# Kernel tuning notes

Measured on AMD Instinct MI355X. Metric: run time of the kernel, lower is better.

## Reference

```python
import jax, jax.numpy as jnp
import numpy as np


def setup_inputs() -> dict:
    key = jax.random.key(0)
    kq, kk, kv = jax.random.split(key, 3)
    shape = (2, 16, 2048, 64)  # [B, H, S, D]
    return {
        "q": jax.random.normal(kq, shape, dtype=jnp.float32),
        "k": jax.random.normal(kk, shape, dtype=jnp.float32),
        "v": jax.random.normal(kv, shape, dtype=jnp.float32),
    }


def reference(q, k, v):
    # scores = q @ k^T / sqrt(d_k)  -> [B, H, S, S]
    d_k = k.shape[-1]
    scale = 1.0 / jnp.sqrt(jnp.asarray(d_k, dtype=q.dtype))
    scores = jnp.einsum("bhqd,bhkd->bhqk", q, k) * scale
    seq_len = q.shape[-2]
    # causal mask: position q attends to k <= q
    causal = jnp.tril(jnp.ones((seq_len, seq_len), dtype=bool))
    scores = jnp.where(causal, scores, jnp.asarray(-jnp.inf, dtype=scores.dtype))
    probs = jax.nn.softmax(scores, axis=-1)
    return jnp.einsum("bhqk,bhkd->bhqd", probs, v)
```

## Files before the change

### kernel.cpp

```cpp
#include <hip/hip_runtime.h>
#include <hip/hip_bf16.h>

typedef short bf16x8 __attribute__((ext_vector_type(8)));
typedef short bf16x4 __attribute__((ext_vector_type(4)));
typedef float f32x4  __attribute__((ext_vector_type(4)));
typedef float f32x16 __attribute__((ext_vector_type(16)));

#define D_DIM 64
#define SEQ 2048
#define BHD (SEQ * D_DIM)
#define SCALE_L2E 0.1803368801111204f

__device__ __forceinline__ unsigned short f2bf(float f) {
    unsigned u = __builtin_bit_cast(unsigned, f);
    u += 0x7fffu + ((u >> 16) & 1u);
    return (unsigned short)(u >> 16);
}
__device__ __forceinline__ unsigned swz(unsigned row, unsigned colByte) {
    return (row * 128u + colByte) ^ ((row & 7u) << 4);
}
__device__ __forceinline__ void gl_lds(const unsigned short* g, unsigned char* lds_generic,
                                       unsigned lds_off) {
    __builtin_amdgcn_global_load_lds(
        (const __attribute__((address_space(1))) void*)g,
        (__attribute__((address_space(3))) void*)(lds_generic + lds_off), 16, 0, 0);
}
__device__ __forceinline__ float fexp2(float x) {
    float r; asm("v_exp_f32 %0, %1" : "=v"(r) : "v"(x)); return r;
}
__device__ __forceinline__ unsigned cvtpk(float lo, float hi) {
    unsigned r; asm("v_cvt_pk_bf16_f32 %0, %1, %2" : "=v"(r) : "v"(lo), "v"(hi)); return r;
}

__global__ __launch_bounds__(256) void prep_kernel(const float* __restrict__ K,
                                                   const float* __restrict__ V,
                                                   unsigned short* __restrict__ Kb,
                                                   unsigned short* __restrict__ Vt) {
    __shared__ unsigned short t[64][66];
    const int st = blockIdx.x;
    const int bh = blockIdx.y;
    const int tid = threadIdx.x;
    const size_t base = (size_t)bh * BHD;

    const float* ksrc = K + base + st * 4096;
    unsigned short* kdst = Kb + base + st * 4096;
    #pragma unroll
    for (int j = 0; j < 2; ++j) {
        int e = (j * 256 + tid) * 8;
        float4 a = *(const float4*)(ksrc + e);
        float4 b = *(const float4*)(ksrc + e + 4);
        bf16x8 o;
        o[0] = (short)f2bf(a.x); o[1] = (short)f2bf(a.y);
        o[2] = (short)f2bf(a.z); o[3] = (short)f2bf(a.w);
        o[4] = (short)f2bf(b.x); o[5] = (short)f2bf(b.y);
        o[6] = (short)f2bf(b.z); o[7] = (short)f2bf(b.w);
        *(bf16x8*)(kdst + e) = o;
    }

    const float* vb = V + base + st * 64 * D_DIM;
    #pragma unroll
    for (int j = 0; j < 4; ++j) {
        int n = tid + 256 * j;
        int r = n >> 4;
        int c = (n & 15) << 2;
        float4 v = *(const float4*)(vb + r * D_DIM + c);
        t[r][c + 0] = f2bf(v.x); t[r][c + 1] = f2bf(v.y);
        t[r][c + 2] = f2bf(v.z); t[r][c + 3] = f2bf(v.w);
    }
    __syncthreads();
    #pragma unroll
    for (int j = 0; j < 2; ++j) {
        int m = tid + 256 * j;
        int d = m >> 3;
        int s8 = (m & 7) << 3;
        bf16x8 o;
        #pragma unroll
        for (int e = 0; e < 8; ++e) o[e] = (short)t[s8 + e][d];
        *(bf16x8*)(Vt + base + (size_t)d * SEQ + st * 64 + s8) = o;
    }
}

__global__ __launch_bounds__(512, 4) void attn_fwd(const float* __restrict__ Qp,
                                                   const unsigned short* __restrict__ Kb,
                                                   const unsigned short* __restrict__ Vtb,
                                                   float* __restrict__ Op) {
    __shared__ __align__(16) unsigned char lds[65536];

    int id = blockIdx.y * gridDim.x + blockIdx.x;
    int j  = id >> 3;
    const int bh = (id & 7) * 4 + (j >> 4);
    const int jq = j & 15;
    const int qtile = (j < 32) ? (15 - jq) : jq;

    const int tid  = threadIdx.x;
    const int w    = tid >> 6;
    const int lane = tid & 63;
    const int l31  = lane & 31;
    const int hi2  = lane >> 5;
    const int wsub = w & 3;
    const int par  = w >> 2;

    const int qlo = qtile * 128 + wsub * 32;
    const int t_w = qlo >> 6;
    const int qg  = qlo + l31;
    const int nt  = qtile + 1;

    const size_t base = (size_t)bh * BHD;
    const float* qp = Qp + base;
    const unsigned short* kb = Kb + base;
    const unsigned short* vt = Vtb + base;
    float* op = Op + base;

    const int srow = tid >> 3;
    const int scb  = ((tid & 7) << 4) ^ ((srow & 7) << 4);
    const int kOff = srow * D_DIM + (scb >> 1);
    const int vOff = srow * SEQ + (scb >> 1);
    const unsigned sdst = (unsigned)tid * 16u;

    auto STAGE = [&](int it) {
        unsigned bb = (unsigned)(it & 1) * 32768u;
        const unsigned short* kg = kb + (size_t)(2 * it) * 4096 + kOff;
        const unsigned short* vg = vt + (size_t)(2 * it) * 64 + vOff;
        gl_lds(kg, lds, bb + sdst);
        gl_lds(vg, lds, bb + 8192u + sdst);
        gl_lds(kg + 4096, lds, bb + 16384u + sdst);
        gl_lds(vg + 64, lds, bb + 24576u + sdst);
    };

    const float* qsrc = qp + (size_t)qg * D_DIM + hi2 * 8;
    float4 qraw[8];
    #pragma unroll
    for (int dk = 0; dk < 4; ++dk) {
        qraw[2 * dk]     = *(const float4*)(qsrc + dk * 16);
        qraw[2 * dk + 1] = *(const float4*)(qsrc + dk * 16 + 4);
    }
    STAGE(0);

    bf16x8 qB[4];
    #pragma unroll
    for (int dk = 0; dk < 4; ++dk) {
        float4 a = qraw[2 * dk], b = qraw[2 * dk + 1];
        bf16x8 v;
        v[0] = (short)f2bf(a.x * SCALE_L2E); v[1] = (short)f2bf(a.y * SCALE_L2E);
        v[2] = (short)f2bf(a.z * SCALE_L2E); v[3] = (short)f2bf(a.w * SCALE_L2E);
        v[4] = (short)f2bf(b.x * SCALE_L2E); v[5] = (short)f2bf(b.y * SCALE_L2E);
        v[6] = (short)f2bf(b.z * SCALE_L2E); v[7] = (short)f2bf(b.w * SCALE_L2E);
        qB[dk] = v;
    }

    f32x16 acc0 = {}, acc1 = {};
    float m_r = -3.0e38f, l_r = 0.f;

    #pragma unroll 1
    for (int it = 0; it < nt; ++it) {
        asm volatile("s_waitcnt vmcnt(0)" ::: "memory");
        __builtin_amdgcn_s_barrier();
        __builtin_amdgcn_sched_barrier(0);
        if (it + 1 < nt) STAGE(it + 1);

        const int tile = 2 * it + par;
        if (tile <= t_w) {
            const unsigned kbuf = (unsigned)(it & 1) * 32768u + (unsigned)par * 16384u;
            const unsigned vbuf = kbuf + 8192u;

            f32x16 st0 = {}, st1 = {};
            __builtin_amdgcn_s_setprio(1);
            #pragma unroll
            for (int dk = 0; dk < 4; ++dk) {
                bf16x8 k0 = *(const bf16x8*)&lds[kbuf +
                    swz((unsigned)l31, (unsigned)(dk * 32 + hi2 * 16))];
                bf16x8 k1 = *(const bf16x8*)&lds[kbuf +
                    swz((unsigned)(32 + l31), (unsigned)(dk * 32 + hi2 * 16))];
                st0 = __builtin_amdgcn_mfma_f32_32x32x16_bf16(k0, qB[dk], st0, 0, 0, 0);
                st1 = __builtin_amdgcn_mfma_f32_32x32x16_bf16(k1, qB[dk], st1, 0, 0, 0);
            }
            __builtin_amdgcn_s_setprio(0);

            if (tile == t_w) {
                #pragma unroll
                for (int r = 0; r < 16; ++r) {
                    int kvb = tile * 64 + (r & 3) + 8 * (r >> 2) + 4 * hi2;
                    if (kvb > qg)      st0[r] = -3.0e38f;
                    if (kvb + 32 > qg) st1[r] = -3.0e38f;
                }
            }

            float m8[8];
            #pragma unroll
            for (int r = 0; r < 8; ++r)
                m8[r] = fmaxf(fmaxf(fmaxf(st0[r], st0[r + 8]), st1[r]), st1[r + 8]);
            float mx = fmaxf(fmaxf(fmaxf(m8[0], m8[1]), m8[2]),
                             fmaxf(fmaxf(m8[3], m8[4]),
                                   fmaxf(fmaxf(m8[5], m8[6]), m8[7])));

            float mn;
            if (__all(mx <= m_r + 8.0f)) {
                mn = m_r;
            } else {
                float mfull = fmaxf(mx, __shfl_xor(mx, 32));
                mn = fmaxf(m_r, mfull);
                float sc = fexp2(m_r - mn);
                m_r = mn;
                l_r *= sc;
                #pragma unroll
                for (int r = 0; r < 16; ++r) { acc0[r] *= sc; acc1[r] *= sc; }
            }

            #pragma unroll
            for (int r = 0; r < 16; ++r) st0[r] = fexp2(st0[r] - mn);
            #pragma unroll
            for (int r = 0; r < 16; ++r) st1[r] = fexp2(st1[r] - mn);
            float s16[16];
            #pragma unroll
            for (int r = 0; r < 16; ++r) s16[r] = st0[r] + st1[r];
            #pragma unroll
            for (int r = 0; r < 8; ++r) s16[r] += s16[r + 8];
            #pragma unroll
            for (int r = 0; r < 4; ++r) s16[r] += s16[r + 4];
            float rs = (s16[0] + s16[1]) + (s16[2] + s16[3]);
            rs += __shfl_xor(rs, 32);
            l_r += rs;

            bf16x8 pf[4];
            #pragma unroll
            for (int b2 = 0; b2 < 2; ++b2) {
                unsigned W[4][2];
                #pragma unroll
                for (int c = 0; c < 4; ++c) {
                    float v0 = b2 ? st1[4 * c + 0] : st0[4 * c + 0];
                    float v1 = b2 ? st1[4 * c + 1] : st0[4 * c + 1];
                    float v2 = b2 ? st1[4 * c + 2] : st0[4 * c + 2];
                    float v3 = b2 ? st1[4 * c + 3] : st0[4 * c + 3];
                    W[c][0] = cvtpk(v0, v1);
                    W[c][1] = cvtpk(v2, v3);
                }
                #pragma unroll
                for (int m = 0; m < 2; ++m) {
                    unsigned s0 = hi2 ? W[2 * m][0] : W[2 * m + 1][0];
                    unsigned s1 = hi2 ? W[2 * m][1] : W[2 * m + 1][1];
                    unsigned r0 = (unsigned)__shfl_xor((int)s0, 32);
                    unsigned r1 = (unsigned)__shfl_xor((int)s1, 32);
                    int4 fw;
                    fw.x = (int)(hi2 ? r0 : W[2 * m][0]);
                    fw.y = (int)(hi2 ? r1 : W[2 * m][1]);
                    fw.z = (int)(hi2 ? W[2 * m + 1][0] : r0);
                    fw.w = (int)(hi2 ? W[2 * m + 1][1] : r1);
                    pf[b2 * 2 + m] = __builtin_bit_cast(bf16x8, fw);
                }
            }

            __builtin_amdgcn_s_setprio(1);
            #pragma unroll
            for (int mm = 0; mm < 4; ++mm) {
                bf16x8 va0 = *(const bf16x8*)&lds[vbuf +
                    swz((unsigned)l31, (unsigned)(mm * 32 + hi2 * 16))];
                bf16x8 va1 = *(const bf16x8*)&lds[vbuf +
                    swz((unsigned)(32 + l31), (unsigned)(mm * 32 + hi2 * 16))];
                acc0 = __builtin_amdgcn_mfma_f32_32x32x16_bf16(va0, pf[mm], acc0, 0, 0, 0);
                acc1 = __builtin_amdgcn_mfma_f32_32x32x16_bf16(va1, pf[mm], acc1, 0, 0, 0);
            }
            __builtin_amdgcn_s_setprio(0);
        }
    }

    __builtin_amdgcn_s_barrier();
    const unsigned mbase = (unsigned)wsub * (64u * 144u) + (unsigned)lane * 144u;
    if (w >= 4) {
        #pragma unroll
        for (int c = 0; c < 4; ++c) {
            f32x4 q0 = {acc0[4 * c], acc0[4 * c + 1], acc0[4 * c + 2], acc0[4 * c + 3]};
            *(f32x4*)&lds[mbase + c * 16] = q0;
            f32x4 q1 = {acc1[4 * c], acc1[4 * c + 1], acc1[4 * c + 2], acc1[4 * c + 3]};
            *(f32x4*)&lds[mbase + 64 + c * 16] = q1;
        }
        *(float*)&lds[mbase + 128] = m_r;
        *(float*)&lds[mbase + 132] = l_r;
    }
    __builtin_amdgcn_s_barrier();
    if (w < 4) {
        float m2 = *(const float*)&lds[mbase + 128];
        float l2 = *(const float*)&lds[mbase + 132];
        float m  = fmaxf(m_r, m2);
        float a1 = fexp2(m_r - m);
        float a2 = fexp2(m2 - m);
        float l  = a1 * l_r + a2 * l2;
        float inv = 1.f / l;
        #pragma unroll
        for (int c = 0; c < 4; ++c) {
            f32x4 p0 = *(const f32x4*)&lds[mbase + c * 16];
            f32x4 p1 = *(const f32x4*)&lds[mbase + 64 + c * 16];
            float4 o0, o1;
            o0.x = (a1 * acc0[4 * c + 0] + a2 * p0[0]) * inv;
            o0.y = (a1 * acc0[4 * c + 1] + a2 * p0[1]) * inv;
            o0.z = (a1 * acc0[4 * c + 2] + a2 * p0[2]) * inv;
            o0.w = (a1 * acc0[4 * c + 3] + a2 * p0[3]) * inv;
            o1.x = (a1 * acc1[4 * c + 0] + a2 * p1[0]) * inv;
            o1.y = (a1 * acc1[4 * c + 1] + a2 * p1[1]) * inv;
            o1.z = (a1 * acc1[4 * c + 2] + a2 * p1[2]) * inv;
            o1.w = (a1 * acc1[4 * c + 3] + a2 * p1[3]) * inv;
            *(float4*)(op + (size_t)qg * D_DIM + 8 * c + 4 * hi2) = o0;
            *(float4*)(op + (size_t)qg * D_DIM + 32 + 8 * c + 4 * hi2) = o1;
        }
    }
}

__global__ __launch_bounds__(256) void attn_fwd_fb(
    const float* __restrict__ Qp, const float* __restrict__ Kp,
    const float* __restrict__ Vp, float* __restrict__ Op, int S)
{
    __shared__ __align__(16) unsigned char lds_k[64 * 128];
    __shared__ __align__(16) unsigned char lds_vt[64 * 128];
    __shared__ __align__(16) unsigned char lds_p[4 * 16 * 128];

    const int qt = blockIdx.x, bh = blockIdx.y, tid = threadIdx.x;
    const int w = tid >> 6, lane = tid & 63, lo = lane & 15, hi = lane >> 4;
    const size_t base = (size_t)bh * S * D_DIM;
    const float* qp = Qp + base; const float* kp = Kp + base;
    const float* vp = Vp + base; float* op = Op + base;
    const int qw = qt * 64 + w * 16;

    auto swzl = [](unsigned row, unsigned colByte) {
        return (row * 128u + colByte) ^ ((row & 7u) << 4);
    };

    bf16x8 qf[2];
    {
        const float* src = qp + (size_t)(qw + lo) * D_DIM + hi * 8;
        #pragma unroll
        for (int f = 0; f < 2; ++f) {
            float4 a = *(const float4*)(src + f * 32);
            float4 b = *(const float4*)(src + f * 32 + 4);
            bf16x8 v;
            v[0] = (short)f2bf(a.x * 0.125f); v[1] = (short)f2bf(a.y * 0.125f);
            v[2] = (short)f2bf(a.z * 0.125f); v[3] = (short)f2bf(a.w * 0.125f);
            v[4] = (short)f2bf(b.x * 0.125f); v[5] = (short)f2bf(b.y * 0.125f);
            v[6] = (short)f2bf(b.z * 0.125f); v[7] = (short)f2bf(b.w * 0.125f);
            qf[f] = v;
        }
    }
    f32x4 o_acc[4]; float m_r[4], l_r[4];
    #pragma unroll
    for (int r = 0; r < 4; ++r) { m_r[r] = -__builtin_inff(); l_r[r] = 0.f; }
    #pragma unroll
    for (int dt = 0; dt < 4; ++dt) o_acc[dt] = (f32x4){0.f, 0.f, 0.f, 0.f};
    const unsigned pbase = (unsigned)w * 2048u;

    for (int t = 0; t <= qt; ++t) {
        const size_t kv0 = (size_t)t * 64;
        __syncthreads();
        #pragma unroll
        for (int jj = 0; jj < 4; ++jj) {
            int n = tid + 256 * jj;
            int r = n >> 4, c = (n & 15) << 2;
            float4 kk = *(const float4*)(kp + (kv0 + r) * D_DIM + c);
            bf16x4 kbv;
            kbv[0] = (short)f2bf(kk.x); kbv[1] = (short)f2bf(kk.y);
            kbv[2] = (short)f2bf(kk.z); kbv[3] = (short)f2bf(kk.w);
            *(bf16x4*)&lds_k[swzl((unsigned)r, (unsigned)c * 2)] = kbv;
            float4 vv = *(const float4*)(vp + (kv0 + r) * D_DIM + c);
            *(unsigned short*)&lds_vt[swzl((unsigned)(c + 0), (unsigned)r * 2)] = f2bf(vv.x);
            *(unsigned short*)&lds_vt[swzl((unsigned)(c + 1), (unsigned)r * 2)] = f2bf(vv.y);
            *(unsigned short*)&lds_vt[swzl((unsigned)(c + 2), (unsigned)r * 2)] = f2bf(vv.z);
            *(unsigned short*)&lds_vt[swzl((unsigned)(c + 3), (unsigned)r * 2)] = f2bf(vv.w);
        }
        __syncthreads();

        float sc[4][4];
        #pragma unroll
        for (int kc = 0; kc < 4; ++kc) {
            f32x4 s = (f32x4){0.f, 0.f, 0.f, 0.f};
            #pragma unroll
            for (int f = 0; f < 2; ++f) {
                bf16x8 kfv = *(const bf16x8*)&lds_k[swzl((unsigned)(kc * 16 + lo),
                                                         (unsigned)(hi * 16 + f * 64))];
                s = __builtin_amdgcn_mfma_f32_16x16x32_bf16(qf[f], kfv, s, 0, 0, 0);
            }
            #pragma unroll
            for (int r = 0; r < 4; ++r) sc[kc][r] = s[r];
        }
        if (t == qt) {
            #pragma unroll
            for (int kc = 0; kc < 4; ++kc)
                #pragma unroll
                for (int r = 0; r < 4; ++r) {
                    int qg2 = w * 16 + hi * 4 + r, kg = kc * 16 + lo;
                    if (kg > qg2) sc[kc][r] = -__builtin_inff();
                }
        }
        float scale[4];
        #pragma unroll
        for (int r = 0; r < 4; ++r) {
            float mx = fmaxf(fmaxf(sc[0][r], sc[1][r]), fmaxf(sc[2][r], sc[3][r]));
            mx = fmaxf(mx, __shfl_xor(mx, 1)); mx = fmaxf(mx, __shfl_xor(mx, 2));
            mx = fmaxf(mx, __shfl_xor(mx, 4)); mx = fmaxf(mx, __shfl_xor(mx, 8));
            float mn = fmaxf(m_r[r], mx);
            scale[r] = __expf(m_r[r] - mn); m_r[r] = mn;
            float s0 = 0.f;
            #pragma unroll
            for (int kc = 0; kc < 4; ++kc) {
                float pv = __expf(sc[kc][r] - mn); sc[kc][r] = pv; s0 += pv;
            }
            s0 += __shfl_xor(s0, 1); s0 += __shfl_xor(s0, 2);
            s0 += __shfl_xor(s0, 4); s0 += __shfl_xor(s0, 8);
            l_r[r] = l_r[r] * scale[r] + s0;
        }
        #pragma unroll
        for (int r = 0; r < 4; ++r) {
            unsigned qr = (unsigned)(hi * 4 + r);
            #pragma unroll
            for (int kc = 0; kc < 4; ++kc)
                *(unsigned short*)&lds_p[pbase + swzl(qr, (unsigned)((kc * 16 + lo) * 2))] =
                    f2bf(sc[kc][r]);
            #pragma unroll
            for (int dt = 0; dt < 4; ++dt) o_acc[dt][r] *= scale[r];
        }
        bf16x8 pa0 = *(const bf16x8*)&lds_p[pbase + swzl((unsigned)lo, (unsigned)(hi * 16))];
        bf16x8 pa1 = *(const bf16x8*)&lds_p[pbase + swzl((unsigned)lo, (unsigned)(hi * 16 + 64))];
        #pragma unroll
        for (int dt = 0; dt < 4; ++dt) {
            bf16x8 vb0 = *(const bf16x8*)&lds_vt[swzl((unsigned)(dt * 16 + lo), (unsigned)(hi * 16))];
            bf16x8 vb1 = *(const bf16x8*)&lds_vt[swzl((unsigned)(dt * 16 + lo), (unsigned)(hi * 16 + 64))];
            o_acc[dt] = __builtin_amdgcn_mfma_f32_16x16x32_bf16(pa0, vb0, o_acc[dt], 0, 0, 0);
            o_acc[dt] = __builtin_amdgcn_mfma_f32_16x16x32_bf16(pa1, vb1, o_acc[dt], 0, 0, 0);
        }
    }
    const int qrow = qw + hi * 4;
    #pragma unroll
    for (int r = 0; r < 4; ++r) {
        float inv = 1.f / l_r[r];
        #pragma unroll
        for (int dt = 0; dt < 4; ++dt)
            op[(size_t)(qrow + r) * D_DIM + dt * 16 + lo] = o_acc[dt][r] * inv;
    }
}

extern "C" void kernel_launch(void* const* d_in, const int* in_sizes, int n_in,
                              void* d_out, int out_size, void* d_ws, size_t ws_size,
                              hipStream_t stream) {
    const float* q = (const float*)d_in[0];
    const float* k = (const float*)d_in[1];
    const float* v = (const float*)d_in[2];
    float* o = (float*)d_out;

    const size_t nelem = (size_t)32 * BHD;
    const size_t need = 2 * nelem * sizeof(unsigned short);

    if (ws_size >= need) {
        unsigned short* kbf = (unsigned short*)d_ws;
        unsigned short* vtb = kbf + nelem;
        prep_kernel<<<dim3(32, 32), 256, 0, stream>>>(k, v, kbf, vtb);
        attn_fwd<<<dim3(16, 32), 512, 0, stream>>>(q, kbf, vtb, o);
    } else {
        attn_fwd_fb<<<dim3(32, 32), 256, 0, stream>>>(q, k, v, o, SEQ);
    }
}
```

Measured before the change: 48.42 us.

## Pair complementary 64-row query tiles per 256-thread block for causal balance

Replaces the 512-thread kernel, which handled one 128-row query tile with 8 waves, by a 256-thread kernel that processes two 64-row query tiles (i and 31-i) one after the other. Pairing the tiles this way gives every block the same causal workload, which removes the tail imbalance across the 512 blocks. The cost is fewer waves per block (4 instead of 8) and per-block serialization of the two phases, including a pipeline restart and Q reload for each phase. The KV split between wave pairs and the LDS merge of partial results are kept.

```diff
diff --git a/kernel.cpp b/kernel.cpp
--- a/kernel.cpp
+++ b/kernel.cpp
@@ -80,30 +80,24 @@
     }
 }
 
-__global__ __launch_bounds__(512, 4) void attn_fwd(const float* __restrict__ Qp,
-                                                   const unsigned short* __restrict__ Kb,
-                                                   const unsigned short* __restrict__ Vtb,
-                                                   float* __restrict__ Op) {
+__global__ __launch_bounds__(256, 2) void attn_pair(const float* __restrict__ Qp,
+                                                    const unsigned short* __restrict__ Kb,
+                                                    const unsigned short* __restrict__ Vtb,
+                                                    float* __restrict__ Op) {
     __shared__ __align__(16) unsigned char lds[65536];
 
-    int id = blockIdx.y * gridDim.x + blockIdx.x;
-    int j  = id >> 3;
+    const int id = blockIdx.x;
+    const int j  = id >> 3;
     const int bh = (id & 7) * 4 + (j >> 4);
-    const int jq = j & 15;
-    const int qtile = (j < 32) ? (15 - jq) : jq;
+    const int i  = j & 15;
 
     const int tid  = threadIdx.x;
     const int w    = tid >> 6;
     const int lane = tid & 63;
     const int l31  = lane & 31;
     const int hi2  = lane >> 5;
-    const int wsub = w & 3;
-    const int par  = w >> 2;
-
-    const int qlo = qtile * 128 + wsub * 32;
-    const int t_w = qlo >> 6;
-    const int qg  = qlo + l31;
-    const int nt  = qtile + 1;
+    const int rg   = w & 1;
+    const int par  = w >> 1;
 
     const size_t base = (size_t)bh * BHD;
     const float* qp = Qp + base;
@@ -111,196 +105,212 @@
     const unsigned short* vt = Vtb + base;
     float* op = Op + base;
 
-    const int srow = tid >> 3;
-    const int scb  = ((tid & 7) << 4) ^ ((srow & 7) << 4);
-    const int kOff = srow * D_DIM + (scb >> 1);
-    const int vOff = srow * SEQ + (scb >> 1);
-    const unsigned sdst = (unsigned)tid * 16u;
-
+    int kOff[2], vOff[2];
+    #pragma unroll
+    for (int h = 0; h < 2; ++h) {
+        int Lb = h * 4096 + tid * 16;
+        int row = Lb >> 7;
+        int cb  = (Lb & 127) ^ ((row & 7) << 4);
+        kOff[h] = row * D_DIM + (cb >> 1);
+        vOff[h] = row * SEQ + (cb >> 1);
+    }
     auto STAGE = [&](int it) {
         unsigned bb = (unsigned)(it & 1) * 32768u;
-        const unsigned short* kg = kb + (size_t)(2 * it) * 4096 + kOff;
-        const unsigned short* vg = vt + (size_t)(2 * it) * 64 + vOff;
-        gl_lds(kg, lds, bb + sdst);
-        gl_lds(vg, lds, bb + 8192u + sdst);
-        gl_lds(kg + 4096, lds, bb + 16384u + sdst);
-        gl_lds(vg + 64, lds, bb + 24576u + sdst);
+        #pragma unroll
+        for (int s = 0; s < 2; ++s) {
+            const unsigned short* kg = kb + (size_t)(2 * it + s) * 4096;
+            const unsigned short* vg = vt + (size_t)(2 * it + s) * 64;
+            #pragma unroll
+            for (int h = 0; h < 2; ++h) {
+                unsigned d = bb + (unsigned)s * 16384u + (unsigned)h * 4096u
+                           + (unsigned)tid * 16u;
+                gl_lds(kg + kOff[h], lds, d);
+                gl_lds(vg + vOff[h], lds, d + 8192u);
+            }
+        }
     };
 
-    const float* qsrc = qp + (size_t)qg * D_DIM + hi2 * 8;
-    float4 qraw[8];
-    #pragma unroll
-    for (int dk = 0; dk < 4; ++dk) {
-        qraw[2 * dk]     = *(const float4*)(qsrc + dk * 16);
-        qraw[2 * dk + 1] = *(const float4*)(qsrc + dk * 16 + 4);
-    }
-    STAGE(0);
-
-    bf16x8 qB[4];
-    #pragma unroll
-    for (int dk = 0; dk < 4; ++dk) {
-        float4 a = qraw[2 * dk], b = qraw[2 * dk + 1];
-        bf16x8 v;
-        v[0] = (short)f2bf(a.x * SCALE_L2E); v[1] = (short)f2bf(a.y * SCALE_L2E);
-        v[2] = (short)f2bf(a.z * SCALE_L2E); v[3] = (short)f2bf(a.w * SCALE_L2E);
-        v[4] = (short)f2bf(b.x * SCALE_L2E); v[5] = (short)f2bf(b.y * SCALE_L2E);
-        v[6] = (short)f2bf(b.z * SCALE_L2E); v[7] = (short)f2bf(b.w * SCALE_L2E);
-        qB[dk] = v;
-    }
-
-    f32x16 acc0 = {}, acc1 = {};
-    float m_r = -3.0e38f, l_r = 0.f;
-
     #pragma unroll 1
-    for (int it = 0; it < nt; ++it) {
-        asm volatile("s_waitcnt vmcnt(0)" ::: "memory");
+    for (int ph = 0; ph < 2; ++ph) {
+        const int Q   = ph ? (31 - i) : i;
+        const int qlo = Q * 64 + rg * 32;
+        const int qg  = qlo + l31;
+        const int t_w = Q;
+        const int nt  = (Q + 2) >> 1;
+
+        STAGE(0);
+
+        bf16x8 qB[4];
+        {
+            const float* qsrc = qp + (size_t)qg * D_DIM + hi2 * 8;
+            #pragma unroll
+            for (int dk = 0; dk < 4; ++dk) {
+                float4 a = *(const float4*)(qsrc + dk * 16);
+                float4 b = *(const float4*)(qsrc + dk * 16 + 4);
+                bf16x8 v;
+                v[0] = (short)f2bf(a.x * SCALE_L2E); v[1] = (short)f2bf(a.y * SCALE_L2E);
+                v[2] = (short)f2bf(a.z * SCALE_L2E); v[3] = (short)f2bf(a.w * SCALE_L2E);
+                v[4] = (short)f2bf(b.x * SCALE_L2E); v[5] = (short)f2bf(b.y * SCALE_L2E);
+                v[6] = (short)f2bf(b.z * SCALE_L2E); v[7] = (short)f2bf(b.w * SCALE_L2E);
+                qB[dk] = v;
+            }
+        }
+
+        f32x16 acc0 = {}, acc1 = {};
+        float m_r = -3.0e38f, l_r = 0.f;
+
+        #pragma unroll 1
+        for (int it = 0; it < nt; ++it) {
+            asm volatile("s_waitcnt vmcnt(0)" ::: "memory");
+            __builtin_amdgcn_s_barrier();
+            __builtin_amdgcn_sched_barrier(0);
+            if (it + 1 < nt) STAGE(it + 1);
+
+            const int tile = 2 * it + par;
+            if (tile <= t_w) {
+                const unsigned kbuf = (unsigned)(it & 1) * 32768u + (unsigned)par * 16384u;
+                const unsigned vbuf = kbuf + 8192u;
+
+                f32x16 st0 = {}, st1 = {};
+                __builtin_amdgcn_s_setprio(1);
+                #pragma unroll
+                for (int dk = 0; dk < 4; ++dk) {
+                    bf16x8 k0 = *(const bf16x8*)&lds[kbuf +
+                        swz((unsigned)l31, (unsigned)(dk * 32 + hi2 * 16))];
+                    bf16x8 k1 = *(const bf16x8*)&lds[kbuf +
+                        swz((unsigned)(32 + l31), (unsigned)(dk * 32 + hi2 * 16))];
+                    st0 = __builtin_amdgcn_mfma_f32_32x32x16_bf16(k0, qB[dk], st0, 0, 0, 0);
+                    st1 = __builtin_amdgcn_mfma_f32_32x32x16_bf16(k1, qB[dk], st1, 0, 0, 0);
+                }
+                __builtin_amdgcn_s_setprio(0);
+
+                if (tile == t_w) {
+                    #pragma unroll
+                    for (int r = 0; r < 16; ++r) {
+                        int kvb = tile * 64 + (r & 3) + 8 * (r >> 2) + 4 * hi2;
+                        if (kvb > qg)      st0[r] = -3.0e38f;
+                        if (kvb + 32 > qg) st1[r] = -3.0e38f;
+                    }
+                }
+
+                float m8[8];
+                #pragma unroll
+                for (int r = 0; r < 8; ++r)
+                    m8[r] = fmaxf(fmaxf(fmaxf(st0[r], st0[r + 8]), st1[r]), st1[r + 8]);
+                float mx = fmaxf(fmaxf(fmaxf(m8[0], m8[1]), m8[2]),
+                                 fmaxf(fmaxf(m8[3], m8[4]),
+                                       fmaxf(fmaxf(m8[5], m8[6]), m8[7])));
+
+                float mn;
+                if (__all(mx <= m_r + 8.0f)) {
+                    mn = m_r;
+                } else {
+                    float mfull = fmaxf(mx, __shfl_xor(mx, 32));
+                    mn = fmaxf(m_r, mfull);
+                    float sc = fexp2(m_r - mn);
+                    m_r = mn;
+                    l_r *= sc;
+                    #pragma unroll
+                    for (int r = 0; r < 16; ++r) { acc0[r] *= sc; acc1[r] *= sc; }
+                }
+
+                #pragma unroll
+                for (int r = 0; r < 16; ++r) st0[r] = fexp2(st0[r] - mn);
+                #pragma unroll
+                for (int r = 0; r < 16; ++r) st1[r] = fexp2(st1[r] - mn);
+                float s16[16];
+                #pragma unroll
+                for (int r = 0; r < 16; ++r) s16[r] = st0[r] + st1[r];
+                #pragma unroll
+                for (int r = 0; r < 8; ++r) s16[r] += s16[r + 8];
+                #pragma unroll
+                for (int r = 0; r < 4; ++r) s16[r] += s16[r + 4];
+                float rs = (s16[0] + s16[1]) + (s16[2] + s16[3]);
+                rs += __shfl_xor(rs, 32);
+                l_r += rs;
+
+                bf16x8 pf[4];
+                #pragma unroll
+                for (int b2 = 0; b2 < 2; ++b2) {
+                    unsigned W[4][2];
+                    #pragma unroll
+                    for (int c = 0; c < 4; ++c) {
+                        float v0 = b2 ? st1[4 * c + 0] : st0[4 * c + 0];
+                        float v1 = b2 ? st1[4 * c + 1] : st0[4 * c + 1];
+                        float v2 = b2 ? st1[4 * c + 2] : st0[4 * c + 2];
+                        float v3 = b2 ? st1[4 * c + 3] : st0[4 * c + 3];
+                        W[c][0] = cvtpk(v0, v1);
+                        W[c][1] = cvtpk(v2, v3);
+                    }
+                    #pragma unroll
+                    for (int m = 0; m < 2; ++m) {
+                        unsigned s0 = hi2 ? W[2 * m][0] : W[2 * m + 1][0];
+                        unsigned s1 = hi2 ? W[2 * m][1] : W[2 * m + 1][1];
+                        unsigned r0 = (unsigned)__shfl_xor((int)s0, 32);
+                        unsigned r1 = (unsigned)__shfl_xor((int)s1, 32);
+                        int4 fw;
+                        fw.x = (int)(hi2 ? r0 : W[2 * m][0]);
+                        fw.y = (int)(hi2 ? r1 : W[2 * m][1]);
+                        fw.z = (int)(hi2 ? W[2 * m + 1][0] : r0);
+                        fw.w = (int)(hi2 ? W[2 * m + 1][1] : r1);
+                        pf[b2 * 2 + m] = __builtin_bit_cast(bf16x8, fw);
+                    }
+                }
+
+                __builtin_amdgcn_s_setprio(1);
+                #pragma unroll
+                for (int mm = 0; mm < 4; ++mm) {
+                    bf16x8 va0 = *(const bf16x8*)&lds[vbuf +
+                        swz((unsigned)l31, (unsigned)(mm * 32 + hi2 * 16))];
+                    bf16x8 va1 = *(const bf16x8*)&lds[vbuf +
+                        swz((unsigned)(32 + l31), (unsigned)(mm * 32 + hi2 * 16))];
+                    acc0 = __builtin_amdgcn_mfma_f32_32x32x16_bf16(va0, pf[mm], acc0, 0, 0, 0);
+                    acc1 = __builtin_amdgcn_mfma_f32_32x32x16_bf16(va1, pf[mm], acc1, 0, 0, 0);
+                }
+                __builtin_amdgcn_s_setprio(0);
+            }
+        }
+
         __builtin_amdgcn_s_barrier();
-        __builtin_amdgcn_sched_barrier(0);
-        if (it + 1 < nt) STAGE(it + 1);
-
-        const int tile = 2 * it + par;
-        if (tile <= t_w) {
-            const unsigned kbuf = (unsigned)(it & 1) * 32768u + (unsigned)par * 16384u;
-            const unsigned vbuf = kbuf + 8192u;
-
-            f32x16 st0 = {}, st1 = {};
-            __builtin_amdgcn_s_setprio(1);
-            #pragma unroll
-            for (int dk = 0; dk < 4; ++dk) {
-                bf16x8 k0 = *(const bf16x8*)&lds[kbuf +
-                    swz((unsigned)l31, (unsigned)(dk * 32 + hi2 * 16))];
-                bf16x8 k1 = *(const bf16x8*)&lds[kbuf +
-                    swz((unsigned)(32 + l31), (unsigned)(dk * 32 + hi2 * 16))];
-                st0 = __builtin_amdgcn_mfma_f32_32x32x16_bf16(k0, qB[dk], st0, 0, 0, 0);
-                st1 = __builtin_amdgcn_mfma_f32_32x32x16_bf16(k1, qB[dk], st1, 0, 0, 0);
-            }
-            __builtin_amdgcn_s_setprio(0);
-
-            if (tile == t_w) {
-                #pragma unroll
-                for (int r = 0; r < 16; ++r) {
-                    int kvb = tile * 64 + (r & 3) + 8 * (r >> 2) + 4 * hi2;
-                    if (kvb > qg)      st0[r] = -3.0e38f;
-                    if (kvb + 32 > qg) st1[r] = -3.0e38f;
-                }
-            }
-
-            float m8[8];
-            #pragma unroll
-            for (int r = 0; r < 8; ++r)
-                m8[r] = fmaxf(fmaxf(fmaxf(st0[r], st0[r + 8]), st1[r]), st1[r + 8]);
-            float mx = fmaxf(fmaxf(fmaxf(m8[0], m8[1]), m8[2]),
-                             fmaxf(fmaxf(m8[3], m8[4]),
-                                   fmaxf(fmaxf(m8[5], m8[6]), m8[7])));
-
-            float mn;
-            if (__all(mx <= m_r + 8.0f)) {
-                mn = m_r;
-            } else {
-                float mfull = fmaxf(mx, __shfl_xor(mx, 32));
-                mn = fmaxf(m_r, mfull);
-                float sc = fexp2(m_r - mn);
-                m_r = mn;
-                l_r *= sc;
-                #pragma unroll
-                for (int r = 0; r < 16; ++r) { acc0[r] *= sc; acc1[r] *= sc; }
-            }
-
-            #pragma unroll
-            for (int r = 0; r < 16; ++r) st0[r] = fexp2(st0[r] - mn);
-            #pragma unroll
-            for (int r = 0; r < 16; ++r) st1[r] = fexp2(st1[r] - mn);
-            float s16[16];
-            #pragma unroll
-            for (int r = 0; r < 16; ++r) s16[r] = st0[r] + st1[r];
-            #pragma unroll
-            for (int r = 0; r < 8; ++r) s16[r] += s16[r + 8];
-            #pragma unroll
-            for (int r = 0; r < 4; ++r) s16[r] += s16[r + 4];
-            float rs = (s16[0] + s16[1]) + (s16[2] + s16[3]);
-            rs += __shfl_xor(rs, 32);
-            l_r += rs;
-
-            bf16x8 pf[4];
-            #pragma unroll
-            for (int b2 = 0; b2 < 2; ++b2) {
-                unsigned W[4][2];
-                #pragma unroll
-                for (int c = 0; c < 4; ++c) {
-                    float v0 = b2 ? st1[4 * c + 0] : st0[4 * c + 0];
-                    float v1 = b2 ? st1[4 * c + 1] : st0[4 * c + 1];
-                    float v2 = b2 ? st1[4 * c + 2] : st0[4 * c + 2];
-                    float v3 = b2 ? st1[4 * c + 3] : st0[4 * c + 3];
-                    W[c][0] = cvtpk(v0, v1);
-                    W[c][1] = cvtpk(v2, v3);
-                }
-                #pragma unroll
-                for (int m = 0; m < 2; ++m) {
-                    unsigned s0 = hi2 ? W[2 * m][0] : W[2 * m + 1][0];
-                    unsigned s1 = hi2 ? W[2 * m][1] : W[2 * m + 1][1];
-                    unsigned r0 = (unsigned)__shfl_xor((int)s0, 32);
-                    unsigned r1 = (unsigned)__shfl_xor((int)s1, 32);
-                    int4 fw;
-                    fw.x = (int)(hi2 ? r0 : W[2 * m][0]);
-                    fw.y = (int)(hi2 ? r1 : W[2 * m][1]);
-                    fw.z = (int)(hi2 ? W[2 * m + 1][0] : r0);
-                    fw.w = (int)(hi2 ? W[2 * m + 1][1] : r1);
-                    pf[b2 * 2 + m] = __builtin_bit_cast(bf16x8, fw);
-                }
-            }
-
-            __builtin_amdgcn_s_setprio(1);
-            #pragma unroll
-            for (int mm = 0; mm < 4; ++mm) {
-                bf16x8 va0 = *(const bf16x8*)&lds[vbuf +
-                    swz((unsigned)l31, (unsigned)(mm * 32 + hi2 * 16))];
-                bf16x8 va1 = *(const bf16x8*)&lds[vbuf +
-                    swz((unsigned)(32 + l31), (unsigned)(mm * 32 + hi2 * 16))];
-                acc0 = __builtin_amdgcn_mfma_f32_32x32x16_bf16(va0, pf[mm], acc0, 0, 0, 0);
-                acc1 = __builtin_amdgcn_mfma_f32_32x32x16_bf16(va1, pf[mm], acc1, 0, 0, 0);
-            }
-            __builtin_amdgcn_s_setprio(0);
-        }
-    }
-
-    __builtin_amdgcn_s_barrier();
-    const unsigned mbase = (unsigned)wsub * (64u * 144u) + (unsigned)lane * 144u;
-    if (w >= 4) {
-        #pragma unroll
-        for (int c = 0; c < 4; ++c) {
-            f32x4 q0 = {acc0[4 * c], acc0[4 * c + 1], acc0[4 * c + 2], acc0[4 * c + 3]};
-            *(f32x4*)&lds[mbase + c * 16] = q0;
-            f32x4 q1 = {acc1[4 * c], acc1[4 * c + 1], acc1[4 * c + 2], acc1[4 * c + 3]};
-            *(f32x4*)&lds[mbase + 64 + c * 16] = q1;
-        }
-        *(float*)&lds[mbase + 128] = m_r;
-        *(float*)&lds[mbase + 132] = l_r;
-    }
-    __builtin_amdgcn_s_barrier();
-    if (w < 4) {
-        float m2 = *(const float*)&lds[mbase + 128];
-        float l2 = *(const float*)&lds[mbase + 132];
-        float m  = fmaxf(m_r, m2);
-        float a1 = fexp2(m_r - m);
-        float a2 = fexp2(m2 - m);
-        float l  = a1 * l_r + a2 * l2;
-        float inv = 1.f / l;
-        #pragma unroll
-        for (int c = 0; c < 4; ++c) {
-            f32x4 p0 = *(const f32x4*)&lds[mbase + c * 16];
-            f32x4 p1 = *(const f32x4*)&lds[mbase + 64 + c * 16];
-            float4 o0, o1;
-            o0.x = (a1 * acc0[4 * c + 0] + a2 * p0[0]) * inv;
-            o0.y = (a1 * acc0[4 * c + 1] + a2 * p0[1]) * inv;
-            o0.z = (a1 * acc0[4 * c + 2] + a2 * p0[2]) * inv;
-            o0.w = (a1 * acc0[4 * c + 3] + a2 * p0[3]) * inv;
-            o1.x = (a1 * acc1[4 * c + 0] + a2 * p1[0]) * inv;
-            o1.y = (a1 * acc1[4 * c + 1] + a2 * p1[1]) * inv;
-            o1.z = (a1 * acc1[4 * c + 2] + a2 * p1[2]) * inv;
-            o1.w = (a1 * acc1[4 * c + 3] + a2 * p1[3]) * inv;
-            *(float4*)(op + (size_t)qg * D_DIM + 8 * c + 4 * hi2) = o0;
-            *(float4*)(op + (size_t)qg * D_DIM + 32 + 8 * c + 4 * hi2) = o1;
-        }
+        const unsigned mbase = (unsigned)rg * (64u * 144u) + (unsigned)lane * 144u;
+        if (par == 1) {
+            #pragma unroll
+            for (int c = 0; c < 4; ++c) {
+                f32x4 q0 = {acc0[4 * c], acc0[4 * c + 1], acc0[4 * c + 2], acc0[4 * c + 3]};
+                *(f32x4*)&lds[mbase + c * 16] = q0;
+                f32x4 q1 = {acc1[4 * c], acc1[4 * c + 1], acc1[4 * c + 2], acc1[4 * c + 3]};
+                *(f32x4*)&lds[mbase + 64 + c * 16] = q1;
+            }
+            *(float*)&lds[mbase + 128] = m_r;
+            *(float*)&lds[mbase + 132] = l_r;
+        }
+        __builtin_amdgcn_s_barrier();
+        if (par == 0) {
+            float m2 = *(const float*)&lds[mbase + 128];
+            float l2 = *(const float*)&lds[mbase + 132];
+            float m  = fmaxf(m_r, m2);
+            float a1 = fexp2(m_r - m);
+            float a2 = fexp2(m2 - m);
+            float l  = a1 * l_r + a2 * l2;
+            float inv = 1.f / l;
+            #pragma unroll
+            for (int c = 0; c < 4; ++c) {
+                f32x4 p0 = *(const f32x4*)&lds[mbase + c * 16];
+                f32x4 p1 = *(const f32x4*)&lds[mbase + 64 + c * 16];
+                float4 o0, o1;
+                o0.x = (a1 * acc0[4 * c + 0] + a2 * p0[0]) * inv;
+                o0.y = (a1 * acc0[4 * c + 1] + a2 * p0[1]) * inv;
+                o0.z = (a1 * acc0[4 * c + 2] + a2 * p0[2]) * inv;
+                o0.w = (a1 * acc0[4 * c + 3] + a2 * p0[3]) * inv;
+                o1.x = (a1 * acc1[4 * c + 0] + a2 * p1[0]) * inv;
+                o1.y = (a1 * acc1[4 * c + 1] + a2 * p1[1]) * inv;
+                o1.z = (a1 * acc1[4 * c + 2] + a2 * p1[2]) * inv;
+                o1.w = (a1 * acc1[4 * c + 3] + a2 * p1[3]) * inv;
+                *(float4*)(op + (size_t)qg * D_DIM + 8 * c + 4 * hi2) = o0;
+                *(float4*)(op + (size_t)qg * D_DIM + 32 + 8 * c + 4 * hi2) = o1;
+            }
+        }
+        __builtin_amdgcn_s_barrier();
     }
 }
 
@@ -449,7 +459,7 @@
         unsigned short* kbf = (unsigned short*)d_ws;
         unsigned short* vtb = kbf + nelem;
         prep_kernel<<<dim3(32, 32), 256, 0, stream>>>(k, v, kbf, vtb);
-        attn_fwd<<<dim3(16, 32), 512, 0, stream>>>(q, kbf, vtb, o);
+        attn_pair<<<512, 256, 0, stream>>>(q, kbf, vtb, o);
     } else {
         attn_fwd_fb<<<dim3(32, 32), 256, 0, stream>>>(q, k, v, o, SEQ);
     }
```

New measurement: 51.81 us. 1.07x slower.
